# Kernel optimization log

Measured on AMD Instinct MI355X. Metric: run time of the kernel, lower is better.

## Reference

```python
import jax, jax.numpy as jnp
import numpy as np

B, S, HID, NH, HD = 2, 2048, 1024, 16, 64
SCALE = 1.0 / np.sqrt(HD)
NEG = -1e9


def _rope_cache(seq_len, dim, base=10000.0):
    inv_freq = 1.0 / (base ** (np.arange(0, dim, 2, dtype=np.float32) / dim))
    t = np.arange(seq_len, dtype=np.float32)
    freqs = np.outer(t, inv_freq)                      # [S, dim/2]
    emb = np.concatenate([freqs, freqs], axis=-1)      # [S, dim]
    return jnp.asarray(np.cos(emb)), jnp.asarray(np.sin(emb))


def _rotate_half(x):
    x1, x2 = jnp.split(x, 2, axis=-1)
    return jnp.concatenate([-x2, x1], axis=-1)


def setup_inputs() -> dict:
    key = jax.random.key(0)
    k0, k1, k2, k3, k4 = jax.random.split(key, 5)
    hidden_states = jax.random.normal(k0, (B, S, HID), jnp.float32)
    Wq = jax.random.normal(k1, (HID, NH * HD), jnp.float32) * 0.02
    Wk = jax.random.normal(k2, (HID, NH * HD), jnp.float32) * 0.02
    Wv = jax.random.normal(k3, (HID, NH * HD), jnp.float32) * 0.02
    Wo = jax.random.normal(k4, (NH * HD, HID), jnp.float32) * 0.02
    causal = jnp.tril(jnp.ones((S, S), bool))
    attention_mask = jnp.broadcast_to(
        jnp.where(causal, 0.0, NEG).astype(jnp.float32)[None, None], (B, 1, S, S))
    position_ids = jnp.broadcast_to(jnp.arange(S, dtype=jnp.int32)[None], (B, S))
    cos, sin = _rope_cache(S, HD)
    return {"hidden_states": hidden_states, "attention_mask": attention_mask,
            "position_ids": position_ids, "cos": cos, "sin": sin,
            "Wq": Wq, "Wk": Wk, "Wv": Wv, "Wo": Wo}


def reference(hidden_states, attention_mask, position_ids, cos, sin, Wq, Wk, Wv, Wo):
    b, s, _ = hidden_states.shape
    def proj(W):  # [B,S,HID] @ [HID,NH*HD] -> [B,NH,S,HD]
        return jnp.einsum('bsh,hd->bsd', hidden_states, W).reshape(b, s, NH, HD).transpose(0, 2, 1, 3)
    q, k, v = proj(Wq), proj(Wk), proj(Wv)
    # RoPE: gather per-position cos/sin -> [B,1,S,HD]
    cos_g = cos[position_ids][:, None]
    sin_g = sin[position_ids][:, None]
    q = q * cos_g + _rotate_half(q) * sin_g
    k = k * cos_g + _rotate_half(k) * sin_g
    scores = jnp.einsum('bhqd,bhkd->bhqk', q, k) * SCALE + attention_mask
    attn = jax.nn.softmax(scores.astype(jnp.float32), axis=-1).astype(q.dtype)
    out = jnp.einsum('bhqk,bhkd->bhqd', attn, v)
    out = out.transpose(0, 2, 1, 3).reshape(b, s, NH * HD)
    return jnp.einsum('bsd,dh->bsh', out, Wo)
```

## Files before the change

kernel.cpp:

```cpp
#include <hip/hip_runtime.h>

typedef __bf16 bf16x8 __attribute__((ext_vector_type(8)));
typedef float  f32x4  __attribute__((ext_vector_type(4)));
typedef unsigned short ushortx8 __attribute__((ext_vector_type(8)));
typedef unsigned short ushortx4 __attribute__((ext_vector_type(4)));

static __device__ __forceinline__ unsigned short f2bf(float f) {
  unsigned int u = __builtin_bit_cast(unsigned int, f);
  u += 0x7FFFu + ((u >> 16) & 1u);
  return (unsigned short)(u >> 16);
}
static __device__ __forceinline__ unsigned short f2bf_fast(float f) {
  unsigned int u = __builtin_bit_cast(unsigned int, f);
  return (unsigned short)((u + 0x8000u) >> 16);
}

#define GLL16(gp, lp) __builtin_amdgcn_global_load_lds(                       \
    (const __attribute__((address_space(1))) void*)(gp),                      \
    (__attribute__((address_space(3))) void*)(lp), 16, 0, 0)

__global__ __launch_bounds__(256) void prep_kernel(const float* __restrict__ X,
                                                   const float* __restrict__ W0,
                                                   const float* __restrict__ W1,
                                                   const float* __restrict__ W2,
                                                   const float* __restrict__ W3,
                                                   unsigned short* __restrict__ Xbf,
                                                   unsigned short* __restrict__ D0,
                                                   unsigned short* __restrict__ D1,
                                                   unsigned short* __restrict__ D2,
                                                   unsigned short* __restrict__ D3) {
  int z = blockIdx.z;
  if (z >= 4) {
    long bid = (long)(z - 4) * 1024 + blockIdx.y * 32 + blockIdx.x;
    int tl = threadIdx.y * 32 + threadIdx.x;
    long i = bid * 2048 + (long)tl * 8;
    float4 f0 = *(const float4*)(X + i);
    float4 f1 = *(const float4*)(X + i + 4);
    ushortx8 u;
    u[0] = f2bf(f0.x); u[1] = f2bf(f0.y); u[2] = f2bf(f0.z); u[3] = f2bf(f0.w);
    u[4] = f2bf(f1.x); u[5] = f2bf(f1.y); u[6] = f2bf(f1.z); u[7] = f2bf(f1.w);
    *(ushortx8*)(Xbf + i) = u;
    return;
  }
  const float* src = (z == 0) ? W0 : (z == 1) ? W1 : (z == 2) ? W2 : W3;
  unsigned short* dst = (z == 0) ? D0 : (z == 1) ? D1 : (z == 2) ? D2 : D3;
  const int R = 1024, C = 1024;
  __shared__ unsigned short t[32][33];
  int c = blockIdx.x * 32 + threadIdx.x;
#pragma unroll
  for (int i = 0; i < 4; ++i) {
    int r = blockIdx.y * 32 + threadIdx.y + i * 8;
    t[threadIdx.y + i * 8][threadIdx.x] = f2bf(src[(size_t)r * C + c]);
  }
  __syncthreads();
  int rr = blockIdx.y * 32 + threadIdx.x;
#pragma unroll
  for (int i = 0; i < 4; ++i) {
    int cc = blockIdx.x * 32 + threadIdx.y + i * 8;
    dst[(size_t)cc * R + rr] = t[threadIdx.x][threadIdx.y + i * 8];
  }
}

__global__ __launch_bounds__(512, 2) void gemm256_kernel(
    const unsigned short* __restrict__ A,
    const unsigned short* __restrict__ BT0,
    const unsigned short* __restrict__ BT1,
    const unsigned short* __restrict__ BT2,
    unsigned short* __restrict__ outQ,
    unsigned short* __restrict__ outK,
    unsigned short* __restrict__ outVT,
    const int* __restrict__ pos_ids,
    const float* __restrict__ cosb,
    const float* __restrict__ sinb) {
  const int K = 1024;
  int id = blockIdx.x * 24 + blockIdx.y;
  int z = id >> 6;
  int r_ = id & 63;
  int n_idx = r_ & 3, m_idx = r_ >> 2;
  const unsigned short* BT = (z == 0) ? BT0 : (z == 1 ? BT1 : BT2);
  int m0 = m_idx * 256, n0 = n_idx * 256;
  int t = threadIdx.x, lane = t & 63, w = t >> 6;
  int wy = w >> 2, wx = w & 3;
  int n16 = lane & 15, quad = lane >> 4;

  __shared__ __align__(16) unsigned short sA[4][256][32];
  __shared__ __align__(16) unsigned short sB[4][256][32];
  __shared__ __align__(16) unsigned short sDummy[512];

  int schunk = (lane & 3) ^ ((lane >> 2) & 3) ^ ((lane >> 4) & 3);
  const unsigned short* gA0 = A + (size_t)(m0 + w * 16 + (lane >> 2)) * K + schunk * 8;
  const unsigned short* gB0 = BT + (size_t)(n0 + w * 16 + (lane >> 2)) * K + schunk * 8;
  const size_t rstep = (size_t)128 * K;
  unsigned short* stA = &sA[0][w * 16][0];
  unsigned short* stB = &sB[0][w * 16][0];

  int cs = (quad ^ (n16 & 3) ^ (n16 >> 2)) * 8;
  const unsigned short* rdA = &sA[0][wy * 128 + n16][0] + cs;
  const unsigned short* rdB = &sB[0][wx * 64 + n16][0] + cs;

  f32x4 acc[8][4];
#pragma unroll
  for (int i = 0; i < 8; ++i)
#pragma unroll
    for (int j = 0; j < 4; ++j) acc[i][j] = f32x4{0.f, 0.f, 0.f, 0.f};

  bf16x8 a[4], b[4];

#define STG_A(tt, d0, d1)                                                             \
  do {                                                                                \
    GLL16(gA0 + (size_t)(tt) * 32, (d0));                                             \
    GLL16(gA0 + (size_t)(tt) * 32 + rstep, (d1));                                     \
  } while (0)
#define STG_B(tt, d0, d1)                                                             \
  do {                                                                                \
    GLL16(gB0 + (size_t)(tt) * 32, (d0));                                             \
    GLL16(gB0 + (size_t)(tt) * 32 + rstep, (d1));                                     \
  } while (0)

#define RD_A4(bufi, mh)                                                               \
  do {                                                                                \
    _Pragma("unroll") for (int i = 0; i < 4; ++i)                                     \
      a[i] = *(const bf16x8*)(rdA + (bufi) * 8192 + ((mh) * 64 + i * 16) * 32);       \
  } while (0)
#define RD_B4(bufi)                                                                   \
  do {                                                                                \
    _Pragma("unroll") for (int jb = 0; jb < 4; ++jb)                                  \
      b[jb] = *(const bf16x8*)(rdB + (bufi) * 8192 + (jb) * 16 * 32);                 \
  } while (0)

#define MMQ(mh, nh)                                                                   \
  do {                                                                                \
    _Pragma("unroll") for (int i = 0; i < 4; ++i)                                     \
      _Pragma("unroll") for (int jj = 0; jj < 2; ++jj)                                \
        acc[(mh) * 4 + i][(nh) * 2 + jj] = __builtin_amdgcn_mfma_f32_16x16x32_bf16(   \
            a[i], b[(nh) * 2 + jj], acc[(mh) * 4 + i][(nh) * 2 + jj], 0, 0, 0);       \
  } while (0)

  STG_A(0, stA, stA + 4096);               STG_B(0, stB, stB + 4096);
  STG_A(1, stA + 8192, stA + 12288);       STG_B(1, stB + 8192, stB + 12288);
  STG_A(2, stA + 16384, stA + 20480);      STG_B(2, stB + 16384, stB + 20480);
  asm volatile("s_waitcnt vmcnt(8)" ::: "memory");
  __builtin_amdgcn_s_barrier();

#pragma unroll 4
  for (int kt = 0; kt < 32; ++kt) {
    int buf = kt & 3;
    int pf = kt + 3;
    bool ok = pf < 32;
    int pfc = ok ? pf : 31;
    unsigned short* dA0 = ok ? (stA + (pf & 3) * 8192) : sDummy;
    unsigned short* dA1 = ok ? (dA0 + 4096) : sDummy;
    unsigned short* dB0 = ok ? (stB + (pf & 3) * 8192) : sDummy;
    unsigned short* dB1 = ok ? (dB0 + 4096) : sDummy;
    RD_A4(buf, 0);
    RD_B4(buf);
    STG_A(pfc, dA0, dA1);
    __builtin_amdgcn_s_barrier();
    __builtin_amdgcn_s_setprio(1);
    MMQ(0, 0); MMQ(0, 1);
    __builtin_amdgcn_s_setprio(0);
    __builtin_amdgcn_sched_barrier(0);
    __builtin_amdgcn_s_barrier();
    RD_A4(buf, 1);
    STG_B(pfc, dB0, dB1);
    __builtin_amdgcn_s_barrier();
    __builtin_amdgcn_s_setprio(1);
    MMQ(1, 0); MMQ(1, 1);
    __builtin_amdgcn_s_setprio(0);
    __builtin_amdgcn_sched_barrier(0);
    asm volatile("s_waitcnt vmcnt(8)" ::: "memory");
    __builtin_amdgcn_s_barrier();
  }
#undef STG_A
#undef STG_B
#undef RD_A4
#undef RD_B4
#undef MMQ

  if (z < 2) {
    const float qs = (z == 0) ? (0.125f * 1.44269504088896340736f) : 1.0f;
#pragma unroll
    for (int mi = 0; mi < 8; ++mi)
#pragma unroll
      for (int r = 0; r < 4; ++r) {
        int row = m0 + wy * 128 + mi * 16 + quad * 4 + r;
        int b_ = row >> 11, s_ = row & 2047;
        int pos = pos_ids[b_ * 2048 + s_];
        const float* cb = cosb + (size_t)pos * 64;
        const float* sb = sinb + (size_t)pos * 64;
#pragma unroll
        for (int ni = 0; ni < 2; ++ni) {
          int d0 = ni * 16 + n16;
          float c0 = cb[d0] * qs, s0 = sb[d0] * qs;
          float c1 = cb[d0 + 32] * qs, s1 = sb[d0 + 32] * qs;
          float x0 = acc[mi][ni][r], x1 = acc[mi][ni + 2][r];
          acc[mi][ni][r]     = x0 * c0 - x1 * s0;
          acc[mi][ni + 2][r] = x1 * c1 + x0 * s1;
        }
      }
    unsigned short* dst = (z == 0) ? outQ : outK;
#pragma unroll
    for (int mi = 0; mi < 8; ++mi)
#pragma unroll
      for (int ni = 0; ni < 4; ++ni)
#pragma unroll
        for (int r = 0; r < 4; ++r) {
          int row = m0 + wy * 128 + mi * 16 + quad * 4 + r;
          int col = n0 + wx * 64 + ni * 16 + n16;
          int b_ = row >> 11, s_ = row & 2047, h_ = col >> 6, d_ = col & 63;
          dst[(((size_t)b_ * 16 + h_) * 2048 + s_) * 64 + d_] = f2bf(acc[mi][ni][r]);
        }
    return;
  }

#pragma unroll
  for (int mi = 0; mi < 8; ++mi)
#pragma unroll
    for (int ni = 0; ni < 4; ++ni) {
      int row = m0 + wy * 128 + mi * 16 + quad * 4;
      int b_ = row >> 11, s_ = row & 2047;
      int col = n0 + wx * 64 + ni * 16 + n16;
      int h_ = col >> 6, d_ = col & 63;
      ushortx4 u;
#pragma unroll
      for (int r = 0; r < 4; ++r) u[r] = f2bf(acc[mi][ni][r]);
      *(ushortx4*)(&outVT[(((size_t)b_ * 16 + h_) * 64 + d_) * 2048 + s_]) = u;
    }
}

__global__ __launch_bounds__(256) void gemm64_kernel(const unsigned short* __restrict__ A,
                                                     const unsigned short* __restrict__ BT,
                                                     float* __restrict__ outF) {
  const int K = 1024, N = 1024;
  int m0 = blockIdx.x * 64, n0 = blockIdx.y * 64;
  int t = threadIdx.x, lane = t & 63, w = t >> 6;
  int wy = w >> 1, wx = w & 1;
  int n16 = lane & 15, quad = lane >> 4;
  __shared__ __align__(16) unsigned short sA0[64 * 32];
  __shared__ __align__(16) unsigned short sA1[64 * 32];
  __shared__ __align__(16) unsigned short sB0[64 * 32];
  __shared__ __align__(16) unsigned short sB1[64 * 32];

  int r4 = lane >> 2, c4 = lane & 3;
  const char* gA = (const char*)(A + (size_t)(m0 + w * 16 + r4) * K) + ((c4 ^ (r4 & 3)) * 16);
  const char* gB = (const char*)(BT + (size_t)(n0 + w * 16 + r4) * K) + ((c4 ^ (r4 & 3)) * 16);

  f32x4 acc[2][2];
#pragma unroll
  for (int i = 0; i < 2; ++i)
#pragma unroll
    for (int j = 0; j < 2; ++j) acc[i][j] = f32x4{0.f, 0.f, 0.f, 0.f};

#define WSTAGE(kk_, SA, SB)                                                     \
  do {                                                                          \
    GLL16(gA + (size_t)(kk_) * 2, SA + (w * 16) * 32);                          \
    GLL16(gB + (size_t)(kk_) * 2, SB + (w * 16) * 32);                          \
  } while (0)

#define WCOMPUTE(SA, SB)                                                        \
  do {                                                                          \
    int cs = (quad ^ (n16 & 3)) * 8;                                            \
    bf16x8 a0 = *(const bf16x8*)(&SA[(wy * 32 + n16) * 32 + cs]);               \
    bf16x8 a1 = *(const bf16x8*)(&SA[(wy * 32 + 16 + n16) * 32 + cs]);          \
    bf16x8 b0 = *(const bf16x8*)(&SB[(wx * 32 + n16) * 32 + cs]);               \
    bf16x8 b1 = *(const bf16x8*)(&SB[(wx * 32 + 16 + n16) * 32 + cs]);          \
    acc[0][0] = __builtin_amdgcn_mfma_f32_16x16x32_bf16(a0, b0, acc[0][0], 0, 0, 0); \
    acc[0][1] = __builtin_amdgcn_mfma_f32_16x16x32_bf16(a0, b1, acc[0][1], 0, 0, 0); \
    acc[1][0] = __builtin_amdgcn_mfma_f32_16x16x32_bf16(a1, b0, acc[1][0], 0, 0, 0); \
    acc[1][1] = __builtin_amdgcn_mfma_f32_16x16x32_bf16(a1, b1, acc[1][1], 0, 0, 0); \
  } while (0)

  WSTAGE(0, sA0, sB0);
  for (int kk = 0; kk < K;) {
    __syncthreads();
    if (kk + 32 < K) WSTAGE(kk + 32, sA1, sB1);
    WCOMPUTE(sA0, sB0);
    kk += 32;
    if (kk >= K) break;
    __syncthreads();
    if (kk + 32 < K) WSTAGE(kk + 32, sA0, sB0);
    WCOMPUTE(sA1, sB1);
    kk += 32;
  }
#undef WSTAGE
#undef WCOMPUTE

#pragma unroll
  for (int mt = 0; mt < 2; ++mt)
#pragma unroll
    for (int nt = 0; nt < 2; ++nt)
#pragma unroll
      for (int r = 0; r < 4; ++r) {
        int row = m0 + wy * 32 + mt * 16 + quad * 4 + r;
        int col = n0 + wx * 32 + nt * 16 + n16;
        outF[(size_t)row * N + col] = acc[mt][nt][r];
      }
}

__global__ __launch_bounds__(512) void attn_kernel(const unsigned short* __restrict__ Q,
                                                   const unsigned short* __restrict__ Kk,
                                                   const unsigned short* __restrict__ VT,
                                                   unsigned short* __restrict__ O) {
  int bh = blockIdx.x;
  int qt = (int)(gridDim.y - 1 - blockIdx.y);
  int t = threadIdx.x;
  int lane = t & 63;
  int w = t >> 6;
  int g = w >> 2;
  int w4 = w & 3;
  int n16 = lane & 15, quad = lane >> 4;
  int r8 = lane >> 3, c8 = lane & 7;
  const unsigned short* Qb = Q + (size_t)bh * 2048 * 64;
  const unsigned short* Kb = Kk + (size_t)bh * 2048 * 64;
  const unsigned short* Vb = VT + (size_t)bh * 64 * 2048;

  __shared__ __align__(16) unsigned short sKV[2 * 2 * 2 * 4096];
  __shared__ __align__(16) unsigned short sP[8][16 * 64];
  unsigned short* spW = sP[w];
  unsigned short* gBase = sKV + g * 16384;

  int b_ = bh >> 4, h_ = bh & 15;
  int nk = qt + 1;
  int u = (nk + 1) >> 1;
  int beg = g ? u : 0;
  int end = g ? nk : u;
  int qg = qt * 64 + w4 * 16 + n16;

  bf16x8 aQ[2];
#pragma unroll
  for (int kb = 0; kb < 2; ++kb)
    aQ[kb] = *(const bf16x8*)(Qb + (size_t)qg * 64 + kb * 32 + quad * 8);

  f32x4 o[4];
  float mst = -3e38f, lst = 0.f;
#pragma unroll
  for (int ct = 0; ct < 4; ++ct) o[ct] = f32x4{0.f, 0.f, 0.f, 0.f};

#define ASTAGE(kt_, BUF)                                                                  \
  do {                                                                                    \
    const unsigned short* kg_ = Kb + (size_t)((kt_) * 64 + w4 * 16) * 64;                 \
    const unsigned short* vg_ = Vb + (size_t)(w4 * 16) * 2048 + (kt_) * 64;               \
    unsigned short* dK = gBase + (BUF) * 8192 + (w4 * 16) * 64;                           \
    unsigned short* dV = dK + 4096;                                                       \
    GLL16(kg_ + (size_t)r8 * 64 + (c8 ^ r8) * 8, dK);                                     \
    GLL16(kg_ + (size_t)(8 + r8) * 64 + (c8 ^ r8) * 8, dK + 8 * 64);                      \
    GLL16(vg_ + (size_t)r8 * 2048 + (c8 ^ r8) * 8, dV);                                   \
    GLL16(vg_ + (size_t)(8 + r8) * 2048 + (c8 ^ r8) * 8, dV + 8 * 64);                    \
  } while (0)

#define ACOMPUTE(kt_, BUF)                                                                \
  do {                                                                                    \
    const unsigned short* kT_ = gBase + (BUF) * 8192;                                     \
    const unsigned short* vT_ = kT_ + 4096;                                               \
    f32x4 sc[4];                                \
    _Pragma("unroll") for (int mt = 0; mt < 4; ++mt) {                                    \
      const unsigned short* kr = &kT_[(mt * 16 + n16) * 64];                              \
      bf16x8 ka0 = *(const bf16x8*)(kr + ((quad ^ (n16 & 7)) * 8));                       \
      bf16x8 ka1 = *(const bf16x8*)(kr + (((4 + quad) ^ (n16 & 7)) * 8));                 \
      f32x4 zv = f32x4{0.f, 0.f, 0.f, 0.f};                                               \
      zv = __builtin_amdgcn_mfma_f32_16x16x32_bf16(ka0, aQ[0], zv, 0, 0, 0);              \
      sc[mt] = __builtin_amdgcn_mfma_f32_16x16x32_bf16(ka1, aQ[1], zv, 0, 0, 0);          \
    }                                                                                     \
    float p[4][4];                                                                        \
    _Pragma("unroll") for (int mt = 0; mt < 4; ++mt)                                      \
      _Pragma("unroll") for (int r = 0; r < 4; ++r) p[mt][r] = sc[mt][r];                 \
    if ((kt_) == nk - 1) {                                 \
      int kb0 = (kt_) * 64 + quad * 4;                                                    \
      _Pragma("unroll") for (int mt = 0; mt < 4; ++mt)                                    \
        _Pragma("unroll") for (int r = 0; r < 4; ++r)                                     \
          if (kb0 + mt * 16 + r > qg) p[mt][r] = -3e38f;                                  \
    }                                                                                     \
    float rm = p[0][0];                                                                   \
    _Pragma("unroll") for (int mt = 0; mt < 4; ++mt)                                      \
      _Pragma("unroll") for (int r = 0; r < 4; ++r) rm = fmaxf(rm, p[mt][r]);             \
    rm = fmaxf(rm, __shfl_xor(rm, 16));                                                   \
    rm = fmaxf(rm, __shfl_xor(rm, 32));                                                   \
    float mn = fmaxf(mst, rm);                                                            \
    float al = exp2f(mst - mn);                                                           \
    mst = mn;                                                                             \
    float rs = 0.f;                                                                       \
    _Pragma("unroll") for (int mt = 0; mt < 4; ++mt)                                      \
      _Pragma("unroll") for (int r = 0; r < 4; ++r) {                                     \
        p[mt][r] = exp2f(p[mt][r] - mn);                                                  \
        rs += p[mt][r];                                                                   \
      }                                                                                   \
    lst = lst * al + rs;                                                                  \
    _Pragma("unroll") for (int ct = 0; ct < 4; ++ct)                                      \
      _Pragma("unroll") for (int r = 0; r < 4; ++r) o[ct][r] *= al;                       \
    _Pragma("unroll") for (int mt = 0; mt < 4; ++mt) {                                    \
      ushortx4 uu;                                                                        \
      _Pragma("unroll") for (int r = 0; r < 4; ++r) uu[r] = f2bf_fast(p[mt][r]);          \
      int ch = (mt * 2 + (quad >> 1)) ^ (n16 & 7);                                        \
      *(ushortx4*)(&spW[n16 * 64 + ch * 8 + (quad & 1) * 4]) = uu;                        \
    }                                                                                     \
    __builtin_amdgcn_s_waitcnt(0xC07F);     \
    bf16x8 aP0 = *(const bf16x8*)(&spW[n16 * 64 + ((quad ^ (n16 & 7)) * 8)]);             \
    bf16x8 aP1 = *(const bf16x8*)(&spW[n16 * 64 + (((4 + quad) ^ (n16 & 7)) * 8)]);       \
    _Pragma("unroll") for (int ct = 0; ct < 4; ++ct) {                                    \
      const unsigned short* vr = &vT_[(ct * 16 + n16) * 64];                              \
      bf16x8 va0 = *(const bf16x8*)(vr + ((quad ^ (n16 & 7)) * 8));                       \
      bf16x8 va1 = *(const bf16x8*)(vr + (((4 + quad) ^ (n16 & 7)) * 8));                 \
      o[ct] = __builtin_amdgcn_mfma_f32_16x16x32_bf16(va0, aP0, o[ct], 0, 0, 0);          \
      o[ct] = __builtin_amdgcn_mfma_f32_16x16x32_bf16(va1, aP1, o[ct], 0, 0, 0);          \
    }                                                                                     \
  } while (0)

  if (beg < end) ASTAGE(beg, 0);
  int it = 0;
  while (it < u) {
    __syncthreads();
    {
      int kt = beg + it;
      if (kt + 1 < end) ASTAGE(kt + 1, 1);
      if (kt < end) ACOMPUTE(kt, 0);
    }
    if (++it >= u) break;
    __syncthreads();
    {
      int kt = beg + it;
      if (kt + 1 < end) ASTAGE(kt + 1, 0);
      if (kt < end) ACOMPUTE(kt, 1);
    }
    ++it;
  }
#undef ASTAGE
#undef ACOMPUTE

  lst += __shfl_xor(lst, 16);
  lst += __shfl_xor(lst, 32);

  __syncthreads();
  float* scratch = (float*)sKV;
  int sidx = (w4 * 64 + lane) * 18;
  if (g == 1) {
#pragma unroll
    for (int ct = 0; ct < 4; ++ct)
#pragma unroll
      for (int r = 0; r < 4; ++r) scratch[sidx + ct * 4 + r] = o[ct][r];
    scratch[sidx + 16] = mst;
    scratch[sidx + 17] = lst;
  }
  __syncthreads();
  if (g == 0) {
    float m1 = scratch[sidx + 16], l1 = scratch[sidx + 17];
    float m = fmaxf(mst, m1);
    float a0 = exp2f(mst - m), a1 = exp2f(m1 - m);
    float inv = 1.0f / (lst * a0 + l1 * a1);
#pragma unroll
    for (int ct = 0; ct < 4; ++ct) {
      ushortx4 uo;
#pragma unroll
      for (int r = 0; r < 4; ++r) {
        float v = (o[ct][r] * a0 + scratch[sidx + ct * 4 + r] * a1) * inv;
        uo[r] = f2bf(v);
      }
      size_t addr = ((size_t)b_ * 2048 + qg) * 1024 + h_ * 64 + ct * 16 + quad * 4;
      *(ushortx4*)(&O[addr]) = uo;
    }
  }
}

extern "C" void kernel_launch(void* const* d_in, const int* in_sizes, int n_in,
                              void* d_out, int out_size, void* d_ws, size_t ws_size,
                              hipStream_t stream) {
  const float* X    = (const float*)d_in[0];
  const int*   pos  = (const int*)d_in[2];
  const float* cosb = (const float*)d_in[3];
  const float* sinb = (const float*)d_in[4];
  const float* Wq   = (const float*)d_in[5];
  const float* Wk   = (const float*)d_in[6];
  const float* Wv   = (const float*)d_in[7];
  const float* Wo   = (const float*)d_in[8];
  float* out = (float*)d_out;

  char* ws = (char*)d_ws;
  const size_t SZ_X = 4096UL * 1024 * 2;
  const size_t SZ_W = 1024UL * 1024 * 2;
  unsigned short* Xbf = (unsigned short*)(ws);
  unsigned short* WTq = (unsigned short*)(ws + SZ_X);
  unsigned short* WTk = (unsigned short*)(ws + SZ_X + SZ_W);
  unsigned short* WTv = (unsigned short*)(ws + SZ_X + 2 * SZ_W);
  unsigned short* WTo = (unsigned short*)(ws + SZ_X + 3 * SZ_W);
  unsigned short* Qbf = (unsigned short*)(ws + SZ_X + 4 * SZ_W);
  unsigned short* Kbf = (unsigned short*)(ws + 2 * SZ_X + 4 * SZ_W);
  unsigned short* VTr = (unsigned short*)(ws + 3 * SZ_X + 4 * SZ_W);
  unsigned short* Obf = (unsigned short*)(ws + 4 * SZ_X + 4 * SZ_W);

  prep_kernel<<<dim3(32, 32, 6), dim3(32, 8), 0, stream>>>(
      X, Wq, Wk, Wv, Wo, Xbf, WTq, WTk, WTv, WTo);

  gemm256_kernel<<<dim3(8, 24), 512, 0, stream>>>(Xbf, WTq, WTk, WTv,
                                                  Qbf, Kbf, VTr,
                                                  pos, cosb, sinb);

  attn_kernel<<<dim3(32, 32), 512, 0, stream>>>(Qbf, Kbf, VTr, Obf);

  gemm64_kernel<<<dim3(64, 16), 256, 0, stream>>>(Obf, WTo, out);
}
```

Measured before the change: 206.0 us.

## Load V directly to registers, halve LDS, and use lazy softmax rescaling

V tiles are now read from global memory straight into registers per iteration instead of being staged through LDS, halving the shared-memory footprint to allow more resident blocks (launch bounds now request 4). The online-softmax rescale of the accumulator and running sum is skipped unless a wave's new max exceeds the stored max by more than 8 (log2 units). This cuts LDS traffic and per-tile exp/multiply work, but the V global loads are issued in the same iteration they are used, which can expose latency, and the lazy threshold slightly weakens the numerical bounds on exponentials.

```diff
diff --git a/kernel.cpp b/kernel.cpp
--- a/kernel.cpp
+++ b/kernel.cpp
@@ -297,10 +297,10 @@
       }
 }
 
-__global__ __launch_bounds__(512) void attn_kernel(const unsigned short* __restrict__ Q,
-                                                   const unsigned short* __restrict__ Kk,
-                                                   const unsigned short* __restrict__ VT,
-                                                   unsigned short* __restrict__ O) {
+__global__ __launch_bounds__(512, 4) void attn_kernel(const unsigned short* __restrict__ Q,
+                                                      const unsigned short* __restrict__ Kk,
+                                                      const unsigned short* __restrict__ VT,
+                                                      unsigned short* __restrict__ O) {
   int bh = blockIdx.x;
   int qt = (int)(gridDim.y - 1 - blockIdx.y);
   int t = threadIdx.x;
@@ -314,10 +314,10 @@
   const unsigned short* Kb = Kk + (size_t)bh * 2048 * 64;
   const unsigned short* Vb = VT + (size_t)bh * 64 * 2048;
 
-  __shared__ __align__(16) unsigned short sKV[2 * 2 * 2 * 4096];
+  __shared__ __align__(16) unsigned short sK[2 * 2 * 4096];
   __shared__ __align__(16) unsigned short sP[8][16 * 64];
   unsigned short* spW = sP[w];
-  unsigned short* gBase = sKV + g * 16384;
+  unsigned short* gBase = sK + g * 8192;
 
   int b_ = bh >> 4, h_ = bh & 15;
   int nk = qt + 1;
@@ -332,26 +332,31 @@
     aQ[kb] = *(const bf16x8*)(Qb + (size_t)qg * 64 + kb * 32 + quad * 8);
 
   f32x4 o[4];
+  bf16x8 va[4][2];
   float mst = -3e38f, lst = 0.f;
 #pragma unroll
   for (int ct = 0; ct < 4; ++ct) o[ct] = f32x4{0.f, 0.f, 0.f, 0.f};
+
+#define ALOADV(kt_)                                                                       \
+  do {                                                                                    \
+    const unsigned short* vr0 = Vb + (size_t)n16 * 2048 + (kt_) * 64 + quad * 8;          \
+    _Pragma("unroll") for (int ct = 0; ct < 4; ++ct) {                                    \
+      va[ct][0] = *(const bf16x8*)(vr0 + (size_t)(ct * 16) * 2048);                       \
+      va[ct][1] = *(const bf16x8*)(vr0 + (size_t)(ct * 16) * 2048 + 32);                  \
+    }                                                                                     \
+  } while (0)
 
 #define ASTAGE(kt_, BUF)                                                                  \
   do {                                                                                    \
     const unsigned short* kg_ = Kb + (size_t)((kt_) * 64 + w4 * 16) * 64;                 \
-    const unsigned short* vg_ = Vb + (size_t)(w4 * 16) * 2048 + (kt_) * 64;               \
-    unsigned short* dK = gBase + (BUF) * 8192 + (w4 * 16) * 64;                           \
-    unsigned short* dV = dK + 4096;                                                       \
+    unsigned short* dK = gBase + (BUF) * 4096 + (w4 * 16) * 64;                           \
     GLL16(kg_ + (size_t)r8 * 64 + (c8 ^ r8) * 8, dK);                                     \
     GLL16(kg_ + (size_t)(8 + r8) * 64 + (c8 ^ r8) * 8, dK + 8 * 64);                      \
-    GLL16(vg_ + (size_t)r8 * 2048 + (c8 ^ r8) * 8, dV);                                   \
-    GLL16(vg_ + (size_t)(8 + r8) * 2048 + (c8 ^ r8) * 8, dV + 8 * 64);                    \
   } while (0)
 
 #define ACOMPUTE(kt_, BUF)                                                                \
   do {                                                                                    \
-    const unsigned short* kT_ = gBase + (BUF) * 8192;                                     \
-    const unsigned short* vT_ = kT_ + 4096;                                               \
+    const unsigned short* kT_ = gBase + (BUF) * 4096;                                     \
     f32x4 sc[4];                                \
     _Pragma("unroll") for (int mt = 0; mt < 4; ++mt) {                                    \
       const unsigned short* kr = &kT_[(mt * 16 + n16) * 64];                              \
@@ -375,18 +380,21 @@
       _Pragma("unroll") for (int r = 0; r < 4; ++r) rm = fmaxf(rm, p[mt][r]);             \
     rm = fmaxf(rm, __shfl_xor(rm, 16));                                                   \
     rm = fmaxf(rm, __shfl_xor(rm, 32));                                                   \
-    float mn = fmaxf(mst, rm);                                                            \
-    float al = exp2f(mst - mn);                                                           \
-    mst = mn;                                                                             \
+    if (!__all(rm <= mst + 8.f)) {        \
+      float mn = fmaxf(mst, rm);                                                          \
+      float al = exp2f(mst - mn);                                                         \
+      mst = mn;                                                                           \
+      lst *= al;                                                                          \
+      _Pragma("unroll") for (int ct = 0; ct < 4; ++ct)                                    \
+        _Pragma("unroll") for (int r = 0; r < 4; ++r) o[ct][r] *= al;                     \
+    }                                                                                     \
     float rs = 0.f;                                                                       \
     _Pragma("unroll") for (int mt = 0; mt < 4; ++mt)                                      \
       _Pragma("unroll") for (int r = 0; r < 4; ++r) {                                     \
-        p[mt][r] = exp2f(p[mt][r] - mn);                                                  \
+        p[mt][r] = exp2f(p[mt][r] - mst);                                                 \
         rs += p[mt][r];                                                                   \
       }                                                                                   \
-    lst = lst * al + rs;                                                                  \
-    _Pragma("unroll") for (int ct = 0; ct < 4; ++ct)                                      \
-      _Pragma("unroll") for (int r = 0; r < 4; ++r) o[ct][r] *= al;                       \
+    lst += rs;                                                                            \
     _Pragma("unroll") for (int mt = 0; mt < 4; ++mt) {                                    \
       ushortx4 uu;                                                                        \
       _Pragma("unroll") for (int r = 0; r < 4; ++r) uu[r] = f2bf_fast(p[mt][r]);          \
@@ -397,11 +405,8 @@
     bf16x8 aP0 = *(const bf16x8*)(&spW[n16 * 64 + ((quad ^ (n16 & 7)) * 8)]);             \
     bf16x8 aP1 = *(const bf16x8*)(&spW[n16 * 64 + (((4 + quad) ^ (n16 & 7)) * 8)]);       \
     _Pragma("unroll") for (int ct = 0; ct < 4; ++ct) {                                    \
-      const unsigned short* vr = &vT_[(ct * 16 + n16) * 64];                              \
-      bf16x8 va0 = *(const bf16x8*)(vr + ((quad ^ (n16 & 7)) * 8));                       \
-      bf16x8 va1 = *(const bf16x8*)(vr + (((4 + quad) ^ (n16 & 7)) * 8));                 \
-      o[ct] = __builtin_amdgcn_mfma_f32_16x16x32_bf16(va0, aP0, o[ct], 0, 0, 0);          \
-      o[ct] = __builtin_amdgcn_mfma_f32_16x16x32_bf16(va1, aP1, o[ct], 0, 0, 0);          \
+      o[ct] = __builtin_amdgcn_mfma_f32_16x16x32_bf16(va[ct][0], aP0, o[ct], 0, 0, 0);    \
+      o[ct] = __builtin_amdgcn_mfma_f32_16x16x32_bf16(va[ct][1], aP1, o[ct], 0, 0, 0);    \
     }                                                                                     \
   } while (0)
 
@@ -411,6 +416,7 @@
     __syncthreads();
     {
       int kt = beg + it;
+      if (kt < end) ALOADV(kt);
       if (kt + 1 < end) ASTAGE(kt + 1, 1);
       if (kt < end) ACOMPUTE(kt, 0);
     }
@@ -418,11 +424,13 @@
     __syncthreads();
     {
       int kt = beg + it;
+      if (kt < end) ALOADV(kt);
       if (kt + 1 < end) ASTAGE(kt + 1, 0);
       if (kt < end) ACOMPUTE(kt, 1);
     }
     ++it;
   }
+#undef ALOADV
 #undef ASTAGE
 #undef ACOMPUTE
 
@@ -430,7 +438,7 @@
   lst += __shfl_xor(lst, 32);
 
   __syncthreads();
-  float* scratch = (float*)sKV;
+  float* scratch = (float*)sK;
   int sidx = (w4 * 64 + lane) * 18;
   if (g == 1) {
 #pragma unroll
```

Result: slower. 240.4 us (+16.7%).
